# Kernel tuning notes

Hardware: AMD Instinct MI355X
Metric: run time of the kernel (lower is better)

Reference implementation:

```python
import jax, jax.numpy as jnp
import numpy as np

B, N, F_IN, F_OUT = 8, 2048, 128, 128


def setup_inputs() -> dict:
    key = jax.random.key(0)
    k1, k2, k3, k4 = jax.random.split(key, 4)
    h = jax.random.normal(k1, (B, N, F_IN), dtype=jnp.float32)
    adj = (jax.random.uniform(k2, (B, N, N)) > 0.5).astype(jnp.float32)
    adj = jnp.maximum(adj, jnp.eye(N, dtype=jnp.float32)[None])
    # torch nn.Linear weights: W is [out_features, in_features], a is [1, 2*out_features]
    W = jax.random.normal(k3, (F_OUT, F_IN), dtype=jnp.float32) * 0.05
    a = jax.random.normal(k4, (1, 2 * F_OUT), dtype=jnp.float32) * 0.05
    return {"h": h, "adj": adj, "W": W, "a": a}


def reference(h, adj, W, a):
    # Wh = W(h): [B, N, F_OUT]
    Wh = jnp.einsum("bnf,of->bno", h, W)
    # attn_fc(concat(Wh_i, Wh_j)) == (Wh_i @ a1) + (Wh_j @ a2): exact split of the
    # linear layer, avoiding the O(B*N*N*2F) concat intermediate.
    a1 = a[0, :F_OUT]
    a2 = a[0, F_OUT:]
    e_i = Wh @ a1  # [B, N]  score contribution of destination node i
    e_j = Wh @ a2  # [B, N]  score contribution of source node j
    e = e_i[:, :, None] + e_j[:, None, :]  # [B, N, N]
    e = e + (1.0 - adj) * (-1e9)
    alpha = jax.nn.softmax(e, axis=-1)  # [B, N, N]
    # weighted aggregation: h_out[b,i] = sum_j alpha[b,i,j] * Wh[b,j]
    h_out = jnp.einsum("bij,bjo->bio", alpha, Wh)
    return h_out
```

## Files before the change

### kernel.cpp

```cpp
#include <hip/hip_runtime.h>
#include <stdint.h>

typedef __bf16 bf16x8 __attribute__((ext_vector_type(8)));
typedef float f32x4 __attribute__((ext_vector_type(4)));
typedef unsigned short u16x8 __attribute__((ext_vector_type(8)));

constexpr int NB = 8;
constexpr int N  = 2048;
constexpr int F  = 128;

__device__ __forceinline__ unsigned short bf16r(float f) {
    unsigned u = __float_as_uint(f);
    return (unsigned short)((u + 0x7FFFu + ((u >> 16) & 1u)) >> 16);
}
__device__ __forceinline__ float bf2f(unsigned short s) {
    return __uint_as_float(((unsigned)s) << 16);
}


__global__ __launch_bounds__(256) void k1_wh(const float* __restrict__ h,
                                             const float* __restrict__ W,
                                             unsigned short* __restrict__ Wb) {
    const int tid  = threadIdx.x;
    const int lane = tid & 63, wid = tid >> 6;
    const int quad = lane >> 4, l15 = lane & 15;
    const int wm = wid >> 1, wn = wid & 1;
    const int m0 = blockIdx.x * 64;
    const int batch = m0 >> 11;
    const int nbase = m0 & 2047;

    f32x4 acc[2][4] = {};

#pragma unroll
    for (int kk = 0; kk < 4; ++kk) {
        const int k = kk * 32 + quad * 8;
        bf16x8 afr[2], bfr[4];
#pragma unroll
        for (int rt = 0; rt < 2; ++rt) {
            const float* src = h + (size_t)(m0 + wm * 32 + rt * 16 + l15) * F + k;
            float4 x0 = *(const float4*)src;
            float4 x1 = *(const float4*)(src + 4);
            afr[rt][0] = (__bf16)x0.x; afr[rt][1] = (__bf16)x0.y;
            afr[rt][2] = (__bf16)x0.z; afr[rt][3] = (__bf16)x0.w;
            afr[rt][4] = (__bf16)x1.x; afr[rt][5] = (__bf16)x1.y;
            afr[rt][6] = (__bf16)x1.z; afr[rt][7] = (__bf16)x1.w;
        }
#pragma unroll
        for (int ct = 0; ct < 4; ++ct) {
            const int o = wn * 64 + ct * 16 + l15;
            const float* src = W + (size_t)o * F + k;
            float4 x0 = *(const float4*)src;
            float4 x1 = *(const float4*)(src + 4);
            bfr[ct][0] = (__bf16)x0.x; bfr[ct][1] = (__bf16)x0.y;
            bfr[ct][2] = (__bf16)x0.z; bfr[ct][3] = (__bf16)x0.w;
            bfr[ct][4] = (__bf16)x1.x; bfr[ct][5] = (__bf16)x1.y;
            bfr[ct][6] = (__bf16)x1.z; bfr[ct][7] = (__bf16)x1.w;
        }
#pragma unroll
        for (int rt = 0; rt < 2; ++rt)
#pragma unroll
            for (int ct = 0; ct < 4; ++ct)
                acc[rt][ct] = __builtin_amdgcn_mfma_f32_16x16x32_bf16(
                    afr[rt], bfr[ct], acc[rt][ct], 0, 0, 0);
    }

#pragma unroll
    for (int rt = 0; rt < 2; ++rt)
#pragma unroll
        for (int ct = 0; ct < 4; ++ct) {
            const int o  = wn * 64 + ct * 16 + l15;
            const int n0 = nbase + wm * 32 + rt * 16 + quad * 4;
            size_t off = (size_t)batch * N * F + (size_t)(n0 >> 3) * 1024 + o * 8 + (n0 & 7);
            ushort4 v;
            v.x = bf16r(acc[rt][ct][0]); v.y = bf16r(acc[rt][ct][1]);
            v.z = bf16r(acc[rt][ct][2]); v.w = bf16r(acc[rt][ct][3]);
            *(ushort4*)&Wb[off] = v;
        }
}

__global__ __launch_bounds__(256) void k2_scale(const unsigned short* __restrict__ Wb,
                                                const float* __restrict__ a,
                                                unsigned short* __restrict__ Wb2,
                                                unsigned short* __restrict__ p16) {
    const int tid  = threadIdx.x;
    const int lane = tid & 63, wid = tid >> 6;
    const int g = blockIdx.x * 4 + wid;
    const int b = g >> 8, grp = g & 255;

    const size_t base = (size_t)b * N * F + (size_t)grp * 1024 + lane * 16;
    bf16x8 v0 = *(const bf16x8*)(Wb + base);
    bf16x8 v1 = *(const bf16x8*)(Wb + base + 8);

    const float a0 = a[F + 2 * lane], a1 = a[F + 2 * lane + 1];
    float part[8];
#pragma unroll
    for (int nn = 0; nn < 8; ++nn)
        part[nn] = (float)v0[nn] * a0 + (float)v1[nn] * a1;

#pragma unroll
    for (int m = 1; m < 64; m <<= 1)
#pragma unroll
        for (int nn = 0; nn < 8; ++nn)
            part[nn] += __shfl_xor(part[nn], m);

    u16x8 pv;
    float pf[8];
#pragma unroll
    for (int nn = 0; nn < 8; ++nn) {
        unsigned short pb = bf16r(expf(part[nn]));
        pv[nn] = pb;
        pf[nn] = bf2f(pb);
    }
    if (lane == 0)
        *(u16x8*)&p16[b * N + grp * 8] = pv;

    bf16x8 w0, w1;
#pragma unroll
    for (int nn = 0; nn < 8; ++nn) {
        w0[nn] = (__bf16)bf2f(bf16r(pf[nn] * (float)v0[nn]));
        w1[nn] = (__bf16)bf2f(bf16r(pf[nn] * (float)v1[nn]));
    }
    *(bf16x8*)(Wb2 + base)     = w0;
    *(bf16x8*)(Wb2 + base + 8) = w1;
}

__global__ __launch_bounds__(256, 2) void k3_attn(const float* __restrict__ adj,
                                                  const unsigned short* __restrict__ Wb2,
                                                  const unsigned short* __restrict__ p16,
                                                  float* __restrict__ out) {
    const int tid  = threadIdx.x;
    const int lane = tid & 63, wid = tid >> 6;
    const int quad = lane >> 4, l15 = lane & 15;
    const int wm = wid >> 1, wn = wid & 1;
    const int b  = blockIdx.x >> 6;
    const int i0 = (blockIdx.x & 63) * 32;

    const float* ar = adj + (size_t)b * N * N + (size_t)(i0 + wm * 16 + l15) * N + quad * 8;
    const char*  bB = (const char*)(Wb2 + (size_t)b * N * F) + quad * 2048 + wn * 1024 + l15 * 16;
    const unsigned short* pq = p16 + b * N + quad * 8;

    f32x4 acc[4] = {};
    f32x4 dacc = {};

    f32x4  xa[8][2];
    bf16x8 xb[2][5];

    auto chunkA = [&](int c, int s) {
        xa[s][0] = __builtin_nontemporal_load((const f32x4*)(ar + c * 32));
        xa[s][1] = __builtin_nontemporal_load((const f32x4*)(ar + c * 32 + 4));
    };
    auto chunkB = [&](int c, int s) {
        const char* p = bB + (size_t)c * 8192;
        xb[s][0] = *(const bf16x8*)(p);
        xb[s][1] = *(const bf16x8*)(p + 256);
        xb[s][2] = *(const bf16x8*)(p + 512);
        xb[s][3] = *(const bf16x8*)(p + 768);
        xb[s][4] = *(const bf16x8*)(pq + c * 32);
    };
    auto compute = [&](int s, int bs) {
        f32x4 x0 = xa[s][0], x1 = xa[s][1];
        bf16x8 af;
        af[0] = (__bf16)x0[0]; af[1] = (__bf16)x0[1];
        af[2] = (__bf16)x0[2]; af[3] = (__bf16)x0[3];
        af[4] = (__bf16)x1[0]; af[5] = (__bf16)x1[1];
        af[6] = (__bf16)x1[2]; af[7] = (__bf16)x1[3];
        acc[0] = __builtin_amdgcn_mfma_f32_16x16x32_bf16(af, xb[bs][0], acc[0], 0, 0, 0);
        acc[1] = __builtin_amdgcn_mfma_f32_16x16x32_bf16(af, xb[bs][1], acc[1], 0, 0, 0);
        acc[2] = __builtin_amdgcn_mfma_f32_16x16x32_bf16(af, xb[bs][2], acc[2], 0, 0, 0);
        acc[3] = __builtin_amdgcn_mfma_f32_16x16x32_bf16(af, xb[bs][3], acc[3], 0, 0, 0);
        dacc   = __builtin_amdgcn_mfma_f32_16x16x32_bf16(af, xb[bs][4], dacc,   0, 0, 0);
    };

#pragma unroll
    for (int d = 0; d < 8; ++d) chunkA(d, d);
    chunkB(0, 0);
    chunkB(1, 1);

    for (int oo = 0; oo < 7; ++oo) {
        const int c0 = oo * 8;
#pragma unroll
        for (int ii = 0; ii < 8; ++ii) {
            compute(ii, ii & 1);
            chunkA(c0 + ii + 8, ii);
            chunkB(c0 + ii + 2, ii & 1);
        }
    }
#pragma unroll
    for (int ii = 0; ii < 8; ++ii) {
        compute(ii, ii & 1);
        if (ii < 6) chunkB(58 + ii, ii & 1);
    }

    float inv[4];
#pragma unroll
    for (int g = 0; g < 4; ++g) inv[g] = 1.0f / dacc[g];

    float* ob = out + (size_t)b * N * F;
#pragma unroll
    for (int ct = 0; ct < 4; ++ct) {
        const int o = wn * 64 + ct * 16 + l15;
#pragma unroll
        for (int g = 0; g < 4; ++g) {
            const int i = i0 + wm * 16 + quad * 4 + g;
            __builtin_nontemporal_store(acc[ct][g] * inv[g], &ob[(size_t)i * F + o]);
        }
    }
}

extern "C" void kernel_launch(void* const* d_in, const int* in_sizes, int n_in,
                              void* d_out, int out_size, void* d_ws, size_t ws_size,
                              hipStream_t stream) {
    const float* h   = (const float*)d_in[0];
    const float* adj = (const float*)d_in[1];
    const float* W   = (const float*)d_in[2];
    const float* a   = (const float*)d_in[3];
    float* out = (float*)d_out;

    unsigned short* Wb  = (unsigned short*)d_ws;
    unsigned short* Wb2 = (unsigned short*)((char*)d_ws + (4u << 20));
    unsigned short* p16 = (unsigned short*)((char*)d_ws + (8u << 20));

    k1_wh<<<NB * N / 64, 256, 0, stream>>>(h, W, Wb);
    k2_scale<<<NB * N / (8 * 4), 256, 0, stream>>>(Wb, a, Wb2, p16);
    k3_attn<<<NB * (N / 32), 256, 0, stream>>>(adj, Wb2, p16, out);
}
```

Before: 252.4 us.

## Restructure attention kernel to 16-row blocks with inline-asm load pipeline

Each block of the attention kernel now covers 16 rows instead of 32, and each wave owns 32 output columns. The grid doubles and the occupancy hint rises to 4 blocks per SM. The old register-buffered prefetch is replaced by a 4-slot software pipeline of inline-asm global loads, with an explicit s_waitcnt vmcnt so more memory requests stay in flight. The aim is to hide the latency of the fp32 adjacency stream. The costs are that each wave now loads the adjacency and p16 data redundantly, the wait-count logic is fragile, and the final iterations clamp to re-load chunk 63.

```diff
diff --git a/kernel.cpp b/kernel.cpp
--- a/kernel.cpp
+++ b/kernel.cpp
@@ -124,72 +124,71 @@
     *(bf16x8*)(Wb2 + base + 8) = w1;
 }
 
-__global__ __launch_bounds__(256, 2) void k3_attn(const float* __restrict__ adj,
+__global__ __launch_bounds__(256, 4) void k3_attn(const float* __restrict__ adj,
                                                   const unsigned short* __restrict__ Wb2,
                                                   const unsigned short* __restrict__ p16,
                                                   float* __restrict__ out) {
     const int tid  = threadIdx.x;
     const int lane = tid & 63, wid = tid >> 6;
     const int quad = lane >> 4, l15 = lane & 15;
-    const int wm = wid >> 1, wn = wid & 1;
-    const int b  = blockIdx.x >> 6;
-    const int i0 = (blockIdx.x & 63) * 32;
-
-    const float* ar = adj + (size_t)b * N * N + (size_t)(i0 + wm * 16 + l15) * N + quad * 8;
-    const char*  bB = (const char*)(Wb2 + (size_t)b * N * F) + quad * 2048 + wn * 1024 + l15 * 16;
-    const unsigned short* pq = p16 + b * N + quad * 8;
-
-    f32x4 acc[4] = {};
+    const int b  = blockIdx.x >> 7;
+    const int i0 = (blockIdx.x & 127) * 16;
+
+    const char* aA = (const char*)adj
+        + ((size_t)b * N * N + (size_t)(i0 + l15) * N) * sizeof(float) + quad * 32;
+    const char* bB = (const char*)Wb2 + (size_t)b * N * F * 2
+        + quad * 2048 + wid * 512 + l15 * 16;
+    const char* pB = (const char*)p16 + (size_t)b * N * 2 + quad * 16;
+
+    f32x4 xa[4][2], xb[4][2], xp[4];
+    f32x4 acc[2] = {};
     f32x4 dacc = {};
 
-    f32x4  xa[8][2];
-    bf16x8 xb[2][5];
-
-    auto chunkA = [&](int c, int s) {
-        xa[s][0] = __builtin_nontemporal_load((const f32x4*)(ar + c * 32));
-        xa[s][1] = __builtin_nontemporal_load((const f32x4*)(ar + c * 32 + 4));
-    };
-    auto chunkB = [&](int c, int s) {
-        const char* p = bB + (size_t)c * 8192;
-        xb[s][0] = *(const bf16x8*)(p);
-        xb[s][1] = *(const bf16x8*)(p + 256);
-        xb[s][2] = *(const bf16x8*)(p + 512);
-        xb[s][3] = *(const bf16x8*)(p + 768);
-        xb[s][4] = *(const bf16x8*)(pq + c * 32);
-    };
-    auto compute = [&](int s, int bs) {
-        f32x4 x0 = xa[s][0], x1 = xa[s][1];
-        bf16x8 af;
-        af[0] = (__bf16)x0[0]; af[1] = (__bf16)x0[1];
-        af[2] = (__bf16)x0[2]; af[3] = (__bf16)x0[3];
-        af[4] = (__bf16)x1[0]; af[5] = (__bf16)x1[1];
-        af[6] = (__bf16)x1[2]; af[7] = (__bf16)x1[3];
-        acc[0] = __builtin_amdgcn_mfma_f32_16x16x32_bf16(af, xb[bs][0], acc[0], 0, 0, 0);
-        acc[1] = __builtin_amdgcn_mfma_f32_16x16x32_bf16(af, xb[bs][1], acc[1], 0, 0, 0);
-        acc[2] = __builtin_amdgcn_mfma_f32_16x16x32_bf16(af, xb[bs][2], acc[2], 0, 0, 0);
-        acc[3] = __builtin_amdgcn_mfma_f32_16x16x32_bf16(af, xb[bs][3], acc[3], 0, 0, 0);
-        dacc   = __builtin_amdgcn_mfma_f32_16x16x32_bf16(af, xb[bs][4], dacc,   0, 0, 0);
-    };
-
-#pragma unroll
-    for (int d = 0; d < 8; ++d) chunkA(d, d);
-    chunkB(0, 0);
-    chunkB(1, 1);
-
-    for (int oo = 0; oo < 7; ++oo) {
-        const int c0 = oo * 8;
-#pragma unroll
-        for (int ii = 0; ii < 8; ++ii) {
-            compute(ii, ii & 1);
-            chunkA(c0 + ii + 8, ii);
-            chunkB(c0 + ii + 2, ii & 1);
-        }
-    }
-#pragma unroll
-    for (int ii = 0; ii < 8; ++ii) {
-        compute(ii, ii & 1);
-        if (ii < 6) chunkB(58 + ii, ii & 1);
-    }
+#define ISSUE(SLOT, CC) do {                                                  \
+    uint64_t _a = (uint64_t)(aA + (size_t)(CC) * 128);                        \
+    uint64_t _b = (uint64_t)(bB + (size_t)(CC) * 8192);                       \
+    uint64_t _p = (uint64_t)(pB + (size_t)(CC) * 64);                         \
+    asm volatile("global_load_dwordx4 %0, %2, off nt\n\t"                     \
+                 "global_load_dwordx4 %1, %2, off offset:16 nt"               \
+        : "=&v"(xa[SLOT][0]), "=&v"(xa[SLOT][1]) : "v"(_a) : "memory");       \
+    asm volatile("global_load_dwordx4 %0, %2, off\n\t"                        \
+                 "global_load_dwordx4 %1, %2, off offset:256"                 \
+        : "=&v"(xb[SLOT][0]), "=&v"(xb[SLOT][1]) : "v"(_b) : "memory");       \
+    asm volatile("global_load_dwordx4 %0, %1, off"                            \
+        : "=&v"(xp[SLOT]) : "v"(_p) : "memory");                              \
+} while (0)
+
+#define STEP(SLOT) do {                                                       \
+    asm volatile("s_waitcnt vmcnt(15)"                                        \
+        : "+v"(xa[SLOT][0]), "+v"(xa[SLOT][1]),                               \
+          "+v"(xb[SLOT][0]), "+v"(xb[SLOT][1]), "+v"(xp[SLOT]) :: "memory");  \
+    f32x4 x0 = xa[SLOT][0], x1 = xa[SLOT][1];                                 \
+    bf16x8 af;                                                                \
+    af[0] = (__bf16)x0[0]; af[1] = (__bf16)x0[1];                             \
+    af[2] = (__bf16)x0[2]; af[3] = (__bf16)x0[3];                             \
+    af[4] = (__bf16)x1[0]; af[5] = (__bf16)x1[1];                             \
+    af[6] = (__bf16)x1[2]; af[7] = (__bf16)x1[3];                             \
+    acc[0] = __builtin_amdgcn_mfma_f32_16x16x32_bf16(                         \
+        af, __builtin_bit_cast(bf16x8, xb[SLOT][0]), acc[0], 0, 0, 0);        \
+    acc[1] = __builtin_amdgcn_mfma_f32_16x16x32_bf16(                         \
+        af, __builtin_bit_cast(bf16x8, xb[SLOT][1]), acc[1], 0, 0, 0);        \
+    dacc   = __builtin_amdgcn_mfma_f32_16x16x32_bf16(                         \
+        af, __builtin_bit_cast(bf16x8, xp[SLOT]), dacc, 0, 0, 0);             \
+} while (0)
+
+    ISSUE(0, 0); ISSUE(1, 1); ISSUE(2, 2); ISSUE(3, 3);
+
+    for (int c = 0; c < 64; c += 4) {
+        int cc;
+        STEP(0); cc = c + 4; if (cc > 63) cc = 63; ISSUE(0, cc);
+        STEP(1); cc = c + 5; if (cc > 63) cc = 63; ISSUE(1, cc);
+        STEP(2); cc = c + 6; if (cc > 63) cc = 63; ISSUE(2, cc);
+        STEP(3); cc = c + 7; if (cc > 63) cc = 63; ISSUE(3, cc);
+    }
+    asm volatile("s_waitcnt vmcnt(0)" ::: "memory");
+
+#undef ISSUE
+#undef STEP
 
     float inv[4];
 #pragma unroll
@@ -197,11 +196,11 @@
 
     float* ob = out + (size_t)b * N * F;
 #pragma unroll
-    for (int ct = 0; ct < 4; ++ct) {
-        const int o = wn * 64 + ct * 16 + l15;
+    for (int ct = 0; ct < 2; ++ct) {
+        const int o = wid * 32 + ct * 16 + l15;
 #pragma unroll
         for (int g = 0; g < 4; ++g) {
-            const int i = i0 + wm * 16 + quad * 4 + g;
+            const int i = i0 + quad * 4 + g;
             __builtin_nontemporal_store(acc[ct][g] * inv[g], &ob[(size_t)i * F + o]);
         }
     }
@@ -222,5 +221,5 @@
 
     k1_wh<<<NB * N / 64, 256, 0, stream>>>(h, W, Wb);
     k2_scale<<<NB * N / (8 * 4), 256, 0, stream>>>(Wb, a, Wb2, p16);
-    k3_attn<<<NB * (N / 32), 256, 0, stream>>>(adj, Wb2, p16, out);
-}
+    k3_attn<<<NB * (N / 16), 256, 0, stream>>>(adj, Wb2, p16, out);
+}
```

Result: slower. 282.7 us (+12.0%).

## Stage adjacency tiles into LDS via async global_load_lds with double buffering

Applied to the files above, without the earlier changes.

Rewrites the attention kernel to copy adjacency rows into a swizzled, double-buffered shared-memory tile using direct global-to-LDS loads, replacing deep register prefetching. Row tiles shrink from 32 to 16 and each wave now owns 32 output columns, allowing higher occupancy. This is meant to hide adjacency-stream latency with less register pressure. In exchange, twice as many blocks re-read the scaled Wh operand, and a block barrier is added per chunk.

```diff
diff --git a/kernel.cpp b/kernel.cpp
--- a/kernel.cpp
+++ b/kernel.cpp
@@ -1,5 +1,8 @@
 #include <hip/hip_runtime.h>
 #include <stdint.h>
+
+#define AS1 __attribute__((address_space(1)))
+#define AS3 __attribute__((address_space(3)))
 
 typedef __bf16 bf16x8 __attribute__((ext_vector_type(8)));
 typedef float f32x4 __attribute__((ext_vector_type(4)));
@@ -124,71 +127,66 @@
     *(bf16x8*)(Wb2 + base + 8) = w1;
 }
 
-__global__ __launch_bounds__(256, 2) void k3_attn(const float* __restrict__ adj,
+__global__ __launch_bounds__(256, 4) void k3_attn(const float* __restrict__ adj,
                                                   const unsigned short* __restrict__ Wb2,
                                                   const unsigned short* __restrict__ p16,
                                                   float* __restrict__ out) {
+    __shared__ __align__(16) float At[2][16 * 128];
+
     const int tid  = threadIdx.x;
     const int lane = tid & 63, wid = tid >> 6;
     const int quad = lane >> 4, l15 = lane & 15;
-    const int wm = wid >> 1, wn = wid & 1;
-    const int b  = blockIdx.x >> 6;
-    const int i0 = (blockIdx.x & 63) * 32;
-
-    const float* ar = adj + (size_t)b * N * N + (size_t)(i0 + wm * 16 + l15) * N + quad * 8;
-    const char*  bB = (const char*)(Wb2 + (size_t)b * N * F) + quad * 2048 + wn * 1024 + l15 * 16;
-    const unsigned short* pq = p16 + b * N + quad * 8;
-
-    f32x4 acc[4] = {};
+    const int b  = blockIdx.x >> 7;
+    const int i0 = (blockIdx.x & 127) * 16;
+
+    const float* adjb = adj + (size_t)b * N * N;
+    const char*  bB   = (const char*)Wb2 + (size_t)b * N * F * 2 + wid * 512 + l15 * 16;
+    const unsigned short* pb = p16 + b * N + quad * 8;
+
+    const int ls16 = lane & 31;
+    const int riB  = wid * 4 + (lane >> 5);
+    auto stage = [&](int buf, int c) {
+#pragma unroll
+        for (int s = 0; s < 2; ++s) {
+            const int ri = riB + s * 2;
+            const int gf = (((ls16 >> 1) ^ ri) << 3) + ((ls16 & 1) << 2);
+            const float* g = adjb + (size_t)(i0 + ri) * N + c * 128 + gf;
+            __builtin_amdgcn_global_load_lds((const AS1 void*)g,
+                (AS3 void*)((char*)&At[buf][0] + wid * 2048 + s * 1024), 16, 0, 0);
+        }
+    };
+
+    f32x4 acc[2] = {};
     f32x4 dacc = {};
 
-    f32x4  xa[8][2];
-    bf16x8 xb[2][5];
-
-    auto chunkA = [&](int c, int s) {
-        xa[s][0] = __builtin_nontemporal_load((const f32x4*)(ar + c * 32));
-        xa[s][1] = __builtin_nontemporal_load((const f32x4*)(ar + c * 32 + 4));
-    };
-    auto chunkB = [&](int c, int s) {
-        const char* p = bB + (size_t)c * 8192;
-        xb[s][0] = *(const bf16x8*)(p);
-        xb[s][1] = *(const bf16x8*)(p + 256);
-        xb[s][2] = *(const bf16x8*)(p + 512);
-        xb[s][3] = *(const bf16x8*)(p + 768);
-        xb[s][4] = *(const bf16x8*)(pq + c * 32);
-    };
-    auto compute = [&](int s, int bs) {
-        f32x4 x0 = xa[s][0], x1 = xa[s][1];
-        bf16x8 af;
-        af[0] = (__bf16)x0[0]; af[1] = (__bf16)x0[1];
-        af[2] = (__bf16)x0[2]; af[3] = (__bf16)x0[3];
-        af[4] = (__bf16)x1[0]; af[5] = (__bf16)x1[1];
-        af[6] = (__bf16)x1[2]; af[7] = (__bf16)x1[3];
-        acc[0] = __builtin_amdgcn_mfma_f32_16x16x32_bf16(af, xb[bs][0], acc[0], 0, 0, 0);
-        acc[1] = __builtin_amdgcn_mfma_f32_16x16x32_bf16(af, xb[bs][1], acc[1], 0, 0, 0);
-        acc[2] = __builtin_amdgcn_mfma_f32_16x16x32_bf16(af, xb[bs][2], acc[2], 0, 0, 0);
-        acc[3] = __builtin_amdgcn_mfma_f32_16x16x32_bf16(af, xb[bs][3], acc[3], 0, 0, 0);
-        dacc   = __builtin_amdgcn_mfma_f32_16x16x32_bf16(af, xb[bs][4], dacc,   0, 0, 0);
-    };
-
-#pragma unroll
-    for (int d = 0; d < 8; ++d) chunkA(d, d);
-    chunkB(0, 0);
-    chunkB(1, 1);
-
-    for (int oo = 0; oo < 7; ++oo) {
-        const int c0 = oo * 8;
-#pragma unroll
-        for (int ii = 0; ii < 8; ++ii) {
-            compute(ii, ii & 1);
-            chunkA(c0 + ii + 8, ii);
-            chunkB(c0 + ii + 2, ii & 1);
-        }
-    }
-#pragma unroll
-    for (int ii = 0; ii < 8; ++ii) {
-        compute(ii, ii & 1);
-        if (ii < 6) chunkB(58 + ii, ii & 1);
+    stage(0, 0);
+
+    for (int c = 0; c < 16; ++c) {
+        const int cur = c & 1;
+        __syncthreads();
+        if (c + 1 < 16) stage(cur ^ 1, c + 1);
+
+#pragma unroll
+        for (int s = 0; s < 4; ++s) {
+            const char* ab = (const char*)&At[cur][0]
+                           + l15 * 512 + (((s * 4 + quad) ^ l15) << 5);
+            f32x4 x0 = *(const f32x4*)ab;
+            f32x4 x1 = *(const f32x4*)(ab + 16);
+            const char* bp = bB + ((size_t)c * 16 + s * 4 + quad) * 2048;
+            bf16x8 b0 = *(const bf16x8*)bp;
+            bf16x8 b1 = *(const bf16x8*)(bp + 256);
+            bf16x8 pv = *(const bf16x8*)(pb + c * 128 + s * 32);
+
+            bf16x8 af;
+            af[0] = (__bf16)x0[0]; af[1] = (__bf16)x0[1];
+            af[2] = (__bf16)x0[2]; af[3] = (__bf16)x0[3];
+            af[4] = (__bf16)x1[0]; af[5] = (__bf16)x1[1];
+            af[6] = (__bf16)x1[2]; af[7] = (__bf16)x1[3];
+
+            acc[0] = __builtin_amdgcn_mfma_f32_16x16x32_bf16(af, b0, acc[0], 0, 0, 0);
+            acc[1] = __builtin_amdgcn_mfma_f32_16x16x32_bf16(af, b1, acc[1], 0, 0, 0);
+            dacc   = __builtin_amdgcn_mfma_f32_16x16x32_bf16(af, pv, dacc, 0, 0, 0);
+        }
     }
 
     float inv[4];
@@ -197,12 +195,12 @@
 
     float* ob = out + (size_t)b * N * F;
 #pragma unroll
-    for (int ct = 0; ct < 4; ++ct) {
-        const int o = wn * 64 + ct * 16 + l15;
+    for (int ct = 0; ct < 2; ++ct) {
+        const int o = wid * 32 + ct * 16 + l15;
 #pragma unroll
         for (int g = 0; g < 4; ++g) {
-            const int i = i0 + wm * 16 + quad * 4 + g;
-            __builtin_nontemporal_store(acc[ct][g] * inv[g], &ob[(size_t)i * F + o]);
+            const int i = i0 + quad * 4 + g;
+            ob[(size_t)i * F + o] = acc[ct][g] * inv[g];
         }
     }
 }
@@ -222,5 +220,5 @@
 
     k1_wh<<<NB * N / 64, 256, 0, stream>>>(h, W, Wb);
     k2_scale<<<NB * N / (8 * 4), 256, 0, stream>>>(Wb, a, Wb2, p16);
-    k3_attn<<<NB * (N / 32), 256, 0, stream>>>(adj, Wb2, p16, out);
-}
+    k3_attn<<<NB * (N / 16), 256, 0, stream>>>(adj, Wb2, p16, out);
+}
```

Result: faster. 227.5 us (-9.9%).
